# Optimization experiments

Measured on AMD Instinct MI355X. Metric: run time of the kernel, lower is better.

## Reference

```python
import jax, jax.numpy as jnp
import numpy as np

E = 768
NH_REG = 6   # num_heads - cultural_heads
NH_CUL = 2   # cultural_heads


def _branch(x, wq, bq, wk, bk, wv, bv, wo, bo, cb, nh, mask_add):
    # x: [B,T,E]; weights stored as [in,out]; cb: [1,nh,1,hd]
    B, T, Edim = x.shape
    hd = Edim // nh
    scale = hd ** -0.5
    q = (x @ wq + bq).reshape(B, T, nh, hd).transpose(0, 2, 1, 3)
    k = (x @ wk + bk).reshape(B, T, nh, hd).transpose(0, 2, 1, 3)
    v = (x @ wv + bv).reshape(B, T, nh, hd).transpose(0, 2, 1, 3)
    q = q + cb  # learned cultural bias added to Q
    scores = jnp.einsum('bhtd,bhsd->bhts', q, k) * scale
    scores = scores + mask_add
    w = jax.nn.softmax(scores, axis=-1)  # dropout omitted (eval mode)
    out = jnp.einsum('bhts,bhsd->bhtd', w, v)
    out = out.transpose(0, 2, 1, 3).reshape(B, T, Edim)
    return out @ wo + bo


def setup_inputs() -> dict:
    key = jax.random.key(0)
    ks = jax.random.split(key, 24)
    B, S = 2, 2048
    d = {
        'hidden_states': jax.random.normal(ks[0], (B, S, E), jnp.float32),
        'cultural_mask': jax.random.normal(ks[1], (B, S, S), jnp.float32),
        'attention_mask': jax.random.normal(ks[2], (B, 1, 1, S), jnp.float32),
    }
    s = E ** -0.5
    names = ['rq_w', 'rk_w', 'rv_w', 'ro_w', 'cq_w', 'ck_w', 'cv_w', 'co_w']
    for i, n in enumerate(names):
        d[n] = jax.random.normal(ks[3 + i], (E, E), jnp.float32) * s
    for i, n in enumerate(['rq_b', 'rk_b', 'rv_b', 'ro_b', 'cq_b', 'ck_b', 'cv_b', 'co_b']):
        d[n] = jax.random.normal(ks[11 + i], (E,), jnp.float32) * 0.02
    d['r_cb'] = jnp.zeros((1, NH_REG, 1, E // NH_REG), jnp.float32)
    d['c_cb'] = jnp.zeros((1, NH_CUL, 1, E // NH_CUL), jnp.float32)
    # NOTE: concat of two branches gives 2E features -> out layer maps 2E -> E
    d['out_w'] = jax.random.normal(ks[19], (2 * E, E), jnp.float32) * (2 * E) ** -0.5
    d['out_b'] = jax.random.normal(ks[20], (E,), jnp.float32) * 0.02
    return d


def reference(hidden_states, cultural_mask, attention_mask,
              rq_w, rk_w, rv_w, ro_w, cq_w, ck_w, cv_w, co_w,
              rq_b, rk_b, rv_b, ro_b, cq_b, ck_b, cv_b, co_b,
              r_cb, c_cb, out_w, out_b):
    # regular branch: attention_mask only
    reg = _branch(hidden_states, rq_w, rq_b, rk_w, rk_b, rv_w, rv_b,
                  ro_w, ro_b, r_cb, NH_REG, attention_mask)
    # cultural branch: cultural_mask (broadcast over heads) + attention_mask
    cmask = cultural_mask[:, None, :, :] + attention_mask
    cul = _branch(hidden_states, cq_w, cq_b, ck_w, ck_b, cv_w, cv_b,
                  co_w, co_b, c_cb, NH_CUL, cmask)
    combined = jnp.concatenate([reg, cul], axis=-1)  # [B,T,2E]
    return combined @ out_w + out_b
```

## Files before the change

kernel.cpp:

```cpp
#include <hip/hip_runtime.h>
#include <hip/hip_bf16.h>

using u16 = unsigned short;
using u32 = unsigned int;
typedef short short8 __attribute__((ext_vector_type(8)));
typedef float f32x4 __attribute__((ext_vector_type(4)));

#define B_  2
#define S_  2048
#define E_  768
#define BS_ 4096

#define L2E_ 1.44269504088896f
#define FML2_ 17.3123404906676f

__device__ __forceinline__ u16 f2bf(float f) {
  __hip_bfloat16 h = __float2bfloat16(f);
  return *reinterpret_cast<u16*>(&h);
}

__device__ __forceinline__ u32 pk2(float a, float b) {
  return (u32)f2bf(a) | ((u32)f2bf(b) << 16);
}

__device__ __forceinline__ void gld16(const void* g, void* l) {
  __builtin_amdgcn_global_load_lds(
      (const __attribute__((address_space(1))) u32*)g,
      (__attribute__((address_space(3))) u32*)l, 16, 0, 0);
}

__device__ __forceinline__ void stage64(const u16* __restrict__ src, int srcStride,
                                        u16* buf, int w, int lane) {
  const int rl = lane >> 3;
  const int cg0 = lane & 7;
#pragma unroll
  for (int it = 0; it < 4; ++it) {
    int r0 = w * 32 + it * 8;
    int row = r0 + rl;
    int cg = cg0 ^ (row & 7);
    gld16(src + (size_t)row * srcStride + cg * 8, buf + r0 * 64 + lane * 8);
  }
}

__device__ __forceinline__ short8 rdfrag64(const u16* buf, int r, int kt, int quad) {
  int slot = (((kt >> 3) + quad) ^ (r & 7)) & 7;
  return *reinterpret_cast<const short8*>(buf + r * 64 + slot * 8);
}

struct PrepP {
  const float* x;  u16* Xb;
  const float* row; const float* cow; u16* Wrc;
  const float* tsrc[7]; u16* tdst[7]; int trows[7];
  const float* rqb; const float* rkb; const float* rvb;
  const float* cqb; const float* ckb; const float* cvb;
  const float* rcb; const float* ccb;
  float* bqkv; float* bzero;
};

__global__ __launch_bounds__(256) void prep_k(PrepP p) {
  const int bid = blockIdx.x, tid = threadIdx.x;
  __shared__ float tsh[32][33];
  if (bid < 3072) {
    int i = bid * 256 + tid;
    float4 v = reinterpret_cast<const float4*>(p.x)[i];
    reinterpret_cast<uint2*>(p.Xb)[i] = make_uint2(pk2(v.x, v.y), pk2(v.z, v.w));
  } else if (bid < 4224) {
    int i = (bid - 3072) * 256 + tid;
    const float* s = (i < 147456) ? p.row : p.cow;
    int k = (i < 147456) ? i : i - 147456;
    float4 v = reinterpret_cast<const float4*>(s)[k];
    reinterpret_cast<uint2*>(p.Wrc)[i] = make_uint2(pk2(v.x, v.y), pk2(v.z, v.w));
  } else if (bid < 8832) {
    int tb = bid - 4224;
    int mi, ty, tx;
    if (tb < 3456) { mi = tb / 576; int r = tb - mi * 576; ty = r / 24; tx = r - ty * 24; }
    else           { int r = tb - 3456; mi = 6; ty = r / 24; tx = r - ty * 24; }
    const float* src = p.tsrc[mi];
    u16* dst = p.tdst[mi];
    const int rows = p.trows[mi];
    const int r0 = ty * 32, c0 = tx * 32;
    const int txx = tid & 31, tyy = tid >> 5;
#pragma unroll
    for (int d = 0; d < 4; ++d) {
      int r = tyy + d * 8;
      tsh[r][txx] = src[(size_t)(r0 + r) * 768 + c0 + txx];
    }
    __syncthreads();
#pragma unroll
    for (int d = 0; d < 4; ++d) {
      int c = tyy + d * 8;
      dst[(size_t)(c0 + c) * rows + r0 + txx] = f2bf(tsh[txx][c]);
    }
  } else {
    int t = (bid - 8832) * 256 + tid;
    if (t < 4608) {
      int seg = t / 768, i = t - seg * 768;
      float v = 0.f;
      if      (seg == 0) v = p.rqb[i] + p.rcb[i];
      else if (seg == 1) v = p.rkb[i];
      else if (seg == 2) v = p.rvb[i];
      else if (seg == 3) v = p.cqb[i] + p.ccb[i];
      else if (seg == 4) v = p.ckb[i];
      else               v = p.cvb[i];
      p.bqkv[t] = v;
    } else if (t < 6144) {
      p.bzero[t - 4608] = 0.f;
    }
  }
}

__global__ __launch_bounds__(256) void bfused_k(
    const u16* __restrict__ outwT, const float* __restrict__ out_b,
    const float* __restrict__ ro_b, const float* __restrict__ co_b,
    float* __restrict__ bfused) {
  __shared__ float rcb[1536];
  const int tid = threadIdx.x, w = tid >> 6, lane = tid & 63;
  for (int i = tid; i < 768; i += 256) {
    rcb[i] = ro_b[i];
    rcb[768 + i] = co_b[i];
  }
  __syncthreads();
  const int of = blockIdx.x * 4 + w;
  const u16* row = outwT + (size_t)of * 1536 + lane * 24;
  const float* rc = rcb + lane * 24;
  float a0 = 0.f, a1 = 0.f, a2 = 0.f, a3 = 0.f;
#pragma unroll
  for (int g = 0; g < 3; ++g) {
    short8 v = *reinterpret_cast<const short8*>(row + g * 8);
    u32 b0 = ((u32)(u16)v[0]) << 16, b1 = ((u32)(u16)v[1]) << 16;
    u32 b2 = ((u32)(u16)v[2]) << 16, b3 = ((u32)(u16)v[3]) << 16;
    u32 b4 = ((u32)(u16)v[4]) << 16, b5 = ((u32)(u16)v[5]) << 16;
    u32 b6 = ((u32)(u16)v[6]) << 16, b7 = ((u32)(u16)v[7]) << 16;
    a0 = fmaf(*reinterpret_cast<float*>(&b0), rc[g * 8 + 0], a0);
    a1 = fmaf(*reinterpret_cast<float*>(&b1), rc[g * 8 + 1], a1);
    a2 = fmaf(*reinterpret_cast<float*>(&b2), rc[g * 8 + 2], a2);
    a3 = fmaf(*reinterpret_cast<float*>(&b3), rc[g * 8 + 3], a3);
    a0 = fmaf(*reinterpret_cast<float*>(&b4), rc[g * 8 + 4], a0);
    a1 = fmaf(*reinterpret_cast<float*>(&b5), rc[g * 8 + 5], a1);
    a2 = fmaf(*reinterpret_cast<float*>(&b6), rc[g * 8 + 6], a2);
    a3 = fmaf(*reinterpret_cast<float*>(&b7), rc[g * 8 + 7], a3);
  }
  float s = (a0 + a1) + (a2 + a3);
  s += __shfl_xor(s, 1);
  s += __shfl_xor(s, 2);
  s += __shfl_xor(s, 4);
  s += __shfl_xor(s, 8);
  s += __shfl_xor(s, 16);
  s += __shfl_xor(s, 32);
  if (lane == 0) bfused[of] = s + out_b[of];
}


template<int MODE>
__global__ __launch_bounds__(256) void gemm_t_k(
    const u16* __restrict__ A, int lda,
    const u16* __restrict__ BT, int ldb,
    const float* __restrict__ bias, int K,
    const u16* __restrict__ A2, int msplit, int bofs,
    void* __restrict__ Cout, int ldc,
    u16* __restrict__ Qr, u16* __restrict__ Kr, u16* __restrict__ Vtr,
    u16* __restrict__ Qc, u16* __restrict__ Kc, u16* __restrict__ Vtc) {
  __shared__ __align__(16) u16 lA[128 * 64];
  __shared__ __align__(16) u16 lB[128 * 64];
  const int tid = threadIdx.x, w = tid >> 6, lane = tid & 63;
  const int quad = lane >> 4, l15 = lane & 15;
  const int m0 = blockIdx.y * 128, n0 = blockIdx.x * 128;
  if (msplit && m0 >= msplit) { A = A2 - (size_t)msplit * lda; BT += bofs; }

  const f32x4 z4 = {0.f, 0.f, 0.f, 0.f};
  f32x4 acc[4][4];
#pragma unroll
  for (int i = 0; i < 4; ++i)
#pragma unroll
    for (int j = 0; j < 4; ++j) acc[i][j] = z4;

  for (int kc = 0; kc < K; kc += 64) {
    stage64(A + (size_t)m0 * lda + kc, lda, lA, w, lane);
    stage64(BT + (size_t)n0 * ldb + kc, ldb, lB, w, lane);
    __syncthreads();
#pragma unroll
    for (int kt = 0; kt < 64; kt += 32) {
      short8 af[4], bg[4];
#pragma unroll
      for (int i = 0; i < 4; ++i)
        af[i] = rdfrag64(lA, (w >> 1) * 64 + i * 16 + l15, kt, quad);
#pragma unroll
      for (int j = 0; j < 4; ++j)
        bg[j] = rdfrag64(lB, (w & 1) * 64 + j * 16 + l15, kt, quad);
#pragma unroll
      for (int i = 0; i < 4; ++i)
#pragma unroll
        for (int j = 0; j < 4; ++j)
          acc[i][j] = __builtin_amdgcn_mfma_f32_16x16x32_bf16(af[i], bg[j], acc[i][j], 0, 0, 0);
    }
    __syncthreads();
  }

  const int seg = (MODE == 2) ? (m0 / 768) : 0;
#pragma unroll
  for (int i = 0; i < 4; ++i) {
    int f = m0 + (w >> 1) * 64 + i * 16 + quad * 4;
    float4 b4 = *reinterpret_cast<const float4*>(bias + f);
#pragma unroll
    for (int j = 0; j < 4; ++j) {
      int t = n0 + (w & 1) * 64 + j * 16 + l15;
      float v0 = acc[i][j][0] + b4.x;
      float v1 = acc[i][j][1] + b4.y;
      float v2 = acc[i][j][2] + b4.z;
      float v3 = acc[i][j][3] + b4.w;
      if (MODE == 0) {
        *reinterpret_cast<uint2*>((u16*)Cout + (size_t)t * ldc + f) =
            make_uint2(pk2(v0, v1), pk2(v2, v3));
      } else if (MODE == 1) {
        *reinterpret_cast<float4*>((float*)Cout + (size_t)t * ldc + f) =
            make_float4(v0, v1, v2, v3);
      } else {
        int b = t >> 11, s = t & 2047;
        int fs = f - seg * 768;
        if (seg == 0) {
          int h = fs >> 7, d = fs & 127;
          *reinterpret_cast<uint2*>(Qr + ((size_t)(b * 6 + h) * 2048 + s) * 128 + d) =
              make_uint2(pk2(v0, v1), pk2(v2, v3));
        } else if (seg == 1) {
          int h = fs >> 7, d = fs & 127;
          *reinterpret_cast<uint2*>(Kr + ((size_t)(b * 6 + h) * 2048 + s) * 128 + d) =
              make_uint2(pk2(v0, v1), pk2(v2, v3));
        } else if (seg == 2) {
          int h = fs >> 7, d = fs & 127;
          u16* vp = Vtr + ((size_t)(b * 6 + h) * 128 + d) * 2048 + s;
          vp[0] = f2bf(v0); vp[2048] = f2bf(v1); vp[4096] = f2bf(v2); vp[6144] = f2bf(v3);
        } else if (seg == 3) {
          int h = fs / 384, d = fs - h * 384;
          *reinterpret_cast<uint2*>(Qc + ((size_t)(b * 2 + h) * 2048 + s) * 384 + d) =
              make_uint2(pk2(v0, v1), pk2(v2, v3));
        } else if (seg == 4) {
          int h = fs / 384, d = fs - h * 384;
          *reinterpret_cast<uint2*>(Kc + ((size_t)(b * 2 + h) * 2048 + s) * 384 + d) =
              make_uint2(pk2(v0, v1), pk2(v2, v3));
        } else {
          int h = fs / 384, d = fs - h * 384;
          u16* vp = Vtc + ((size_t)(b * 2 + h) * 384 + d) * 2048 + s;
          vp[0] = f2bf(v0); vp[2048] = f2bf(v1); vp[4096] = f2bf(v2); vp[6144] = f2bf(v3);
        }
      }
    }
  }
}

__global__ __launch_bounds__(256) void attn_g1_k(
    const u16* __restrict__ Qr, const u16* __restrict__ Kr,
    const u16* __restrict__ Qc, const u16* __restrict__ Kc,
    u16* __restrict__ Pr, u16* __restrict__ Pc, float* __restrict__ Lp,
    const float* __restrict__ am, const float* __restrict__ cmask,
    float sReg, float sCul, int zoff) {
  __shared__ __align__(16) u16 lA[128 * 64];
  __shared__ __align__(16) u16 lB[128 * 64];
  const int tid = threadIdx.x, w = tid >> 6, lane = tid & 63;
  const int quad = lane >> 4, l15 = lane & 15;
  const int m0 = blockIdx.y * 128, n0 = blockIdx.x * 128;
  const int gz = zoff + blockIdx.z;
  const u16 *A, *BT;
  u16* P;
  const float* cm = nullptr;
  float scl;
  int K, b;
  if (gz < 12) {
    A = Kr + (size_t)gz * S_ * 128;
    BT = Qr + (size_t)gz * S_ * 128;
    K = 128;
    P = Pr + (size_t)blockIdx.z * (size_t)S_ * S_;
    scl = sReg;
    b = gz / 6;
  } else {
    int hc = gz - 12;
    A = Kc + (size_t)hc * S_ * 384;
    BT = Qc + (size_t)hc * S_ * 384;
    K = 384;
    P = Pc + (size_t)hc * (size_t)S_ * S_;
    b = hc >> 1;
    cm = cmask + (size_t)b * S_ * S_;
    scl = sCul;
  }

  const f32x4 z4 = {0.f, 0.f, 0.f, 0.f};
  f32x4 acc[4][4];
#pragma unroll
  for (int i = 0; i < 4; ++i)
#pragma unroll
    for (int j = 0; j < 4; ++j) acc[i][j] = z4;

  for (int kc = 0; kc < K; kc += 64) {
    stage64(A + (size_t)m0 * K + kc, K, lA, w, lane);
    stage64(BT + (size_t)n0 * K + kc, K, lB, w, lane);
    __syncthreads();
#pragma unroll
    for (int kt = 0; kt < 64; kt += 32) {
      short8 af[4], bg[4];
#pragma unroll
      for (int i = 0; i < 4; ++i)
        af[i] = rdfrag64(lA, (w >> 1) * 64 + i * 16 + l15, kt, quad);
#pragma unroll
      for (int j = 0; j < 4; ++j)
        bg[j] = rdfrag64(lB, (w & 1) * 64 + j * 16 + l15, kt, quad);
#pragma unroll
      for (int i = 0; i < 4; ++i)
#pragma unroll
        for (int j = 0; j < 4; ++j)
          acc[i][j] = __builtin_amdgcn_mfma_f32_16x16x32_bf16(af[i], bg[j], acc[i][j], 0, 0, 0);
    }
    __syncthreads();
  }

  const float* amb = am + b * S_;
  float lsum[4] = {0.f, 0.f, 0.f, 0.f};
#pragma unroll
  for (int i = 0; i < 4; ++i) {
    int kb = m0 + (w >> 1) * 64 + i * 16 + quad * 4;
    float4 a4 = *reinterpret_cast<const float4*>(amb + kb);
    float pre0 = fmaf(a4.x, L2E_, -FML2_);
    float pre1 = fmaf(a4.y, L2E_, -FML2_);
    float pre2 = fmaf(a4.z, L2E_, -FML2_);
    float pre3 = fmaf(a4.w, L2E_, -FML2_);
#pragma unroll
    for (int j = 0; j < 4; ++j) {
      int q = n0 + (w & 1) * 64 + j * 16 + l15;
      float c0 = pre0, c1 = pre1, c2 = pre2, c3 = pre3;
      if (cm) {
        float4 cmv = *reinterpret_cast<const float4*>(cm + (size_t)q * S_ + kb);
        c0 = fmaf(cmv.x, L2E_, c0);
        c1 = fmaf(cmv.y, L2E_, c1);
        c2 = fmaf(cmv.z, L2E_, c2);
        c3 = fmaf(cmv.w, L2E_, c3);
      }
      float p0 = exp2f(fmaf(acc[i][j][0], scl, c0));
      float p1 = exp2f(fmaf(acc[i][j][1], scl, c1));
      float p2 = exp2f(fmaf(acc[i][j][2], scl, c2));
      float p3 = exp2f(fmaf(acc[i][j][3], scl, c3));
      lsum[j] += (p0 + p1) + (p2 + p3);
      *reinterpret_cast<uint2*>(P + (size_t)q * S_ + kb) =
          make_uint2(pk2(p0, p1), pk2(p2, p3));
    }
  }
#pragma unroll
  for (int j = 0; j < 4; ++j) {
    float s = lsum[j];
    s += __shfl_xor(s, 16);
    s += __shfl_xor(s, 32);
    if (lane < 16)
      Lp[(size_t)gz * (32 * S_) + ((size_t)((m0 >> 7) * 2 + (w >> 1))) * S_ +
         n0 + (w & 1) * 64 + j * 16 + lane] = s;
  }
}

__global__ __launch_bounds__(256) void attn_g2_k(
    const u16* __restrict__ Pr, const u16* __restrict__ Pc,
    const u16* __restrict__ Vtr, const u16* __restrict__ Vtc,
    const float* __restrict__ Lp, u16* __restrict__ AO, int zoff) {
  const int gz = zoff + blockIdx.z;
  const int m0 = blockIdx.y * 128, n0 = blockIdx.x * 128;
  const u16 *A, *BT;
  int b, colbase;
  if (gz < 12) {
    if (blockIdx.y) return;
    A = Vtr + (size_t)gz * 128 * S_;
    BT = Pr + (size_t)blockIdx.z * (size_t)S_ * S_;
    b = gz / 6;
    colbase = (gz % 6) * 128;
  } else {
    int hc = gz - 12;
    A = Vtc + (size_t)hc * 384 * S_;
    BT = Pc + (size_t)hc * (size_t)S_ * S_;
    b = hc >> 1;
    colbase = 768 + (hc & 1) * 384;
  }
  __shared__ __align__(16) u16 lA[128 * 64];
  __shared__ __align__(16) u16 lB[128 * 64];
  __shared__ float lL[128];
  const int tid = threadIdx.x, w = tid >> 6, lane = tid & 63;
  const int quad = lane >> 4, l15 = lane & 15;

  if (tid < 128) {
    const float* lp = Lp + (size_t)gz * (32 * S_) + (n0 + tid);
    float s = 0.f;
#pragma unroll
    for (int g = 0; g < 32; ++g) s += lp[(size_t)g * S_];
    lL[tid] = 1.f / s;
  }

  const f32x4 z4 = {0.f, 0.f, 0.f, 0.f};
  f32x4 acc[4][4];
#pragma unroll
  for (int i = 0; i < 4; ++i)
#pragma unroll
    for (int j = 0; j < 4; ++j) acc[i][j] = z4;

  for (int kc = 0; kc < S_; kc += 64) {
    stage64(A + (size_t)m0 * S_ + kc, S_, lA, w, lane);
    stage64(BT + (size_t)n0 * S_ + kc, S_, lB, w, lane);
    __syncthreads();
#pragma unroll
    for (int kt = 0; kt < 64; kt += 32) {
      short8 af[4], bg[4];
#pragma unroll
      for (int i = 0; i < 4; ++i)
        af[i] = rdfrag64(lA, (w >> 1) * 64 + i * 16 + l15, kt, quad);
#pragma unroll
      for (int j = 0; j < 4; ++j)
        bg[j] = rdfrag64(lB, (w & 1) * 64 + j * 16 + l15, kt, quad);
#pragma unroll
      for (int i = 0; i < 4; ++i)
#pragma unroll
        for (int j = 0; j < 4; ++j)
          acc[i][j] = __builtin_amdgcn_mfma_f32_16x16x32_bf16(af[i], bg[j], acc[i][j], 0, 0, 0);
    }
    __syncthreads();
  }

  float invl[4];
#pragma unroll
  for (int j = 0; j < 4; ++j) invl[j] = lL[(w & 1) * 64 + j * 16 + l15];
#pragma unroll
  for (int i = 0; i < 4; ++i) {
    int feat = colbase + m0 + (w >> 1) * 64 + i * 16 + quad * 4;
#pragma unroll
    for (int j = 0; j < 4; ++j) {
      int q = n0 + (w & 1) * 64 + j * 16 + l15;
      float v0 = acc[i][j][0] * invl[j];
      float v1 = acc[i][j][1] * invl[j];
      float v2 = acc[i][j][2] * invl[j];
      float v3 = acc[i][j][3] * invl[j];
      *reinterpret_cast<uint2*>(AO + ((size_t)(b * S_ + q)) * 1536 + feat) =
          make_uint2(pk2(v0, v1), pk2(v2, v3));
    }
  }
}


extern "C" void kernel_launch(void* const* d_in, const int* in_sizes, int n_in,
                              void* d_out, int out_size, void* d_ws, size_t ws_size,
                              hipStream_t stream) {
  const float* x     = (const float*)d_in[0];
  const float* cmask = (const float*)d_in[1];
  const float* amask = (const float*)d_in[2];
  const float* W[8]  = { (const float*)d_in[3], (const float*)d_in[4], (const float*)d_in[5],
                         (const float*)d_in[6], (const float*)d_in[7], (const float*)d_in[8],
                         (const float*)d_in[9], (const float*)d_in[10] };
  const float* rq_b = (const float*)d_in[11];
  const float* rk_b = (const float*)d_in[12];
  const float* rv_b = (const float*)d_in[13];
  const float* ro_b = (const float*)d_in[14];
  const float* cq_b = (const float*)d_in[15];
  const float* ck_b = (const float*)d_in[16];
  const float* cv_b = (const float*)d_in[17];
  const float* co_b = (const float*)d_in[18];
  const float* r_cb = (const float*)d_in[19];
  const float* c_cb = (const float*)d_in[20];
  const float* out_w = (const float*)d_in[21];
  const float* out_b = (const float*)d_in[22];

  char* p = (char*)d_ws;
  auto carve = [&](size_t bytes) -> void* {
    void* r = (void*)p;
    p += (bytes + 255) & ~(size_t)255;
    return r;
  };
  u16* Xb    = (u16*)carve((size_t)BS_ * E_ * 2);
  u16* WqkvT = (u16*)carve((size_t)4608 * 768 * 2);
  u16* outwT = (u16*)carve((size_t)768 * 1536 * 2);
  u16* Wrc   = (u16*)carve((size_t)1536 * 768 * 2);
  u16* WfT   = (u16*)carve((size_t)768 * 1536 * 2);
  float* bqkv   = (float*)carve(4608 * 4);
  float* bzero  = (float*)carve(1536 * 4);
  float* bfused = (float*)carve(768 * 4);
  u16* Qr  = (u16*)carve((size_t)B_ * 6 * S_ * 128 * 2);
  u16* Kr  = (u16*)carve((size_t)B_ * 6 * S_ * 128 * 2);
  u16* Vtr = (u16*)carve((size_t)B_ * 6 * S_ * 128 * 2);
  u16* Qc  = (u16*)carve((size_t)B_ * 2 * S_ * 384 * 2);
  u16* Kc  = (u16*)carve((size_t)B_ * 2 * S_ * 384 * 2);
  u16* Vtc = (u16*)carve((size_t)B_ * 2 * S_ * 384 * 2);
  u16* AO  = (u16*)carve((size_t)BS_ * 1536 * 2);

  float* Lp = (float*)Xb;
  u16* Pcul = (u16*)carve((size_t)4 * S_ * S_ * 2);
  size_t used = (size_t)(p - (char*)d_ws);
  size_t rem = (ws_size > used) ? (ws_size - used) : 0;
  int RCH;
  if      (rem >= (size_t)12 * S_ * S_ * 2 + 4096) RCH = 12;
  else if (rem >= (size_t)4  * S_ * S_ * 2 + 4096) RCH = 4;
  else                                             RCH = 2;
  u16* Preg = (u16*)carve((size_t)RCH * S_ * S_ * 2);

  const float sReg = 0.08838834764831845f * L2E_;
  const float sCul = 0.05103103630798288f * L2E_;

  PrepP pp;
  pp.x = x; pp.Xb = Xb;
  pp.row = W[3]; pp.cow = W[7]; pp.Wrc = Wrc;
  const int wsel[6] = {0, 1, 2, 4, 5, 6};
  for (int i = 0; i < 6; ++i) {
    pp.tsrc[i] = W[wsel[i]];
    pp.tdst[i] = WqkvT + (size_t)i * 768 * 768;
    pp.trows[i] = 768;
  }
  pp.tsrc[6] = out_w; pp.tdst[6] = outwT; pp.trows[6] = 1536;
  pp.rqb = rq_b; pp.rkb = rk_b; pp.rvb = rv_b;
  pp.cqb = cq_b; pp.ckb = ck_b; pp.cvb = cv_b;
  pp.rcb = r_cb; pp.ccb = c_cb;
  pp.bqkv = bqkv; pp.bzero = bzero;
  prep_k<<<dim3(8856), 256, 0, stream>>>(pp);

  bfused_k<<<dim3(192), 256, 0, stream>>>(outwT, out_b, ro_b, co_b, bfused);

  gemm_t_k<0><<<dim3(6, 12), 256, 0, stream>>>(
      Wrc, 768, outwT, 1536, bzero, 768,
      Wrc + (size_t)768 * 768, 768, 768, (void*)WfT, 1536,
      nullptr, nullptr, nullptr, nullptr, nullptr, nullptr);

  gemm_t_k<2><<<dim3(32, 36), 256, 0, stream>>>(
      WqkvT, 768, Xb, 768, bqkv, 768,
      (const u16*)nullptr, 0, 0, (void*)nullptr, 0,
      Qr, Kr, Vtr, Qc, Kc, Vtc);

  if (RCH == 12) {
    attn_g1_k<<<dim3(16, 16, 16), 256, 0, stream>>>(
        Qr, Kr, Qc, Kc, Preg, Pcul, Lp, amask, cmask, sReg, sCul, 0);
    attn_g2_k<<<dim3(16, 3, 16), 256, 0, stream>>>(
        Preg, Pcul, Vtr, Vtc, Lp, AO, 0);
  } else {
    attn_g1_k<<<dim3(16, 16, 4), 256, 0, stream>>>(
        Qr, Kr, Qc, Kc, Preg, Pcul, Lp, amask, cmask, sReg, sCul, 12);
    attn_g2_k<<<dim3(16, 3, 4), 256, 0, stream>>>(
        Preg, Pcul, Vtr, Vtc, Lp, AO, 12);
    for (int c = 0; c < 12; c += RCH) {
      attn_g1_k<<<dim3(16, 16, RCH), 256, 0, stream>>>(
          Qr, Kr, Qc, Kc, Preg, Pcul, Lp, amask, cmask, sReg, sCul, c);
      attn_g2_k<<<dim3(16, 1, RCH), 256, 0, stream>>>(
          Preg, Pcul, Vtr, Vtc, Lp, AO, c);
    }
  }

  gemm_t_k<1><<<dim3(32, 6), 256, 0, stream>>>(
      WfT, 1536, AO, 1536, bfused, 1536,
      (const u16*)nullptr, 0, 0, d_out, 768,
      nullptr, nullptr, nullptr, nullptr, nullptr, nullptr);
}
```

Measured before the change: 379.0 us.

## Double-buffer LDS staging in GEMMs and tile the P matrix layout

Adds a double-buffered LDS pipeline to the small GEMMs and the P·V attention kernel, so the next 64-wide K chunk is loaded while MFMAs run on the current one. The probability matrix P is now stored in 128-column key blocks, so each block's rows are contiguous and the P·V kernel reads contiguous 256-byte rows instead of rows strided by S. The MFMA inner loop moves into a shared helper. Double buffering doubles LDS use per block, which may lower occupancy.

```diff
diff --git a/kernel.cpp b/kernel.cpp
--- a/kernel.cpp
+++ b/kernel.cpp
@@ -45,6 +45,26 @@
 __device__ __forceinline__ short8 rdfrag64(const u16* buf, int r, int kt, int quad) {
   int slot = (((kt >> 3) + quad) ^ (r & 7)) & 7;
   return *reinterpret_cast<const short8*>(buf + r * 64 + slot * 8);
+}
+
+__device__ __forceinline__ void mfma_chunk64(const u16* lA, const u16* lB,
+                                             f32x4 (&acc)[4][4],
+                                             int w, int l15, int quad) {
+#pragma unroll
+  for (int kt = 0; kt < 64; kt += 32) {
+    short8 af[4], bg[4];
+#pragma unroll
+    for (int i = 0; i < 4; ++i)
+      af[i] = rdfrag64(lA, (w >> 1) * 64 + i * 16 + l15, kt, quad);
+#pragma unroll
+    for (int j = 0; j < 4; ++j)
+      bg[j] = rdfrag64(lB, (w & 1) * 64 + j * 16 + l15, kt, quad);
+#pragma unroll
+    for (int i = 0; i < 4; ++i)
+#pragma unroll
+      for (int j = 0; j < 4; ++j)
+        acc[i][j] = __builtin_amdgcn_mfma_f32_16x16x32_bf16(af[i], bg[j], acc[i][j], 0, 0, 0);
+  }
 }
 
 struct PrepP {
@@ -151,7 +171,7 @@
 }
 
 
-template<int MODE>
+template<int MODE, int DB>
 __global__ __launch_bounds__(256) void gemm_t_k(
     const u16* __restrict__ A, int lda,
     const u16* __restrict__ BT, int ldb,
@@ -160,8 +180,8 @@
     void* __restrict__ Cout, int ldc,
     u16* __restrict__ Qr, u16* __restrict__ Kr, u16* __restrict__ Vtr,
     u16* __restrict__ Qc, u16* __restrict__ Kc, u16* __restrict__ Vtc) {
-  __shared__ __align__(16) u16 lA[128 * 64];
-  __shared__ __align__(16) u16 lB[128 * 64];
+  __shared__ __align__(16) u16 lA[DB + 1][128 * 64];
+  __shared__ __align__(16) u16 lB[DB + 1][128 * 64];
   const int tid = threadIdx.x, w = tid >> 6, lane = tid & 63;
   const int quad = lane >> 4, l15 = lane & 15;
   const int m0 = blockIdx.y * 128, n0 = blockIdx.x * 128;
@@ -174,26 +194,29 @@
 #pragma unroll
     for (int j = 0; j < 4; ++j) acc[i][j] = z4;
 
-  for (int kc = 0; kc < K; kc += 64) {
-    stage64(A + (size_t)m0 * lda + kc, lda, lA, w, lane);
-    stage64(BT + (size_t)n0 * ldb + kc, ldb, lB, w, lane);
+  if constexpr (DB) {
+    stage64(A + (size_t)m0 * lda, lda, lA[0], w, lane);
+    stage64(BT + (size_t)n0 * ldb, ldb, lB[0], w, lane);
     __syncthreads();
-#pragma unroll
-    for (int kt = 0; kt < 64; kt += 32) {
-      short8 af[4], bg[4];
-#pragma unroll
-      for (int i = 0; i < 4; ++i)
-        af[i] = rdfrag64(lA, (w >> 1) * 64 + i * 16 + l15, kt, quad);
-#pragma unroll
-      for (int j = 0; j < 4; ++j)
-        bg[j] = rdfrag64(lB, (w & 1) * 64 + j * 16 + l15, kt, quad);
-#pragma unroll
-      for (int i = 0; i < 4; ++i)
-#pragma unroll
-        for (int j = 0; j < 4; ++j)
-          acc[i][j] = __builtin_amdgcn_mfma_f32_16x16x32_bf16(af[i], bg[j], acc[i][j], 0, 0, 0);
-    }
-    __syncthreads();
+    int cur = 0;
+    const int nt = K >> 6;
+    for (int t = 0; t < nt; ++t) {
+      if (t + 1 < nt) {
+        stage64(A + (size_t)m0 * lda + (t + 1) * 64, lda, lA[cur ^ 1], w, lane);
+        stage64(BT + (size_t)n0 * ldb + (t + 1) * 64, ldb, lB[cur ^ 1], w, lane);
+      }
+      mfma_chunk64(lA[cur], lB[cur], acc, w, l15, quad);
+      __syncthreads();
+      cur ^= 1;
+    }
+  } else {
+    for (int kc = 0; kc < K; kc += 64) {
+      stage64(A + (size_t)m0 * lda + kc, lda, lA[0], w, lane);
+      stage64(BT + (size_t)n0 * ldb + kc, ldb, lB[0], w, lane);
+      __syncthreads();
+      mfma_chunk64(lA[0], lB[0], acc, w, l15, quad);
+      __syncthreads();
+    }
   }
 
   const int seg = (MODE == 2) ? (m0 / 768) : 0;
@@ -293,29 +316,17 @@
     stage64(A + (size_t)m0 * K + kc, K, lA, w, lane);
     stage64(BT + (size_t)n0 * K + kc, K, lB, w, lane);
     __syncthreads();
-#pragma unroll
-    for (int kt = 0; kt < 64; kt += 32) {
-      short8 af[4], bg[4];
-#pragma unroll
-      for (int i = 0; i < 4; ++i)
-        af[i] = rdfrag64(lA, (w >> 1) * 64 + i * 16 + l15, kt, quad);
-#pragma unroll
-      for (int j = 0; j < 4; ++j)
-        bg[j] = rdfrag64(lB, (w & 1) * 64 + j * 16 + l15, kt, quad);
-#pragma unroll
-      for (int i = 0; i < 4; ++i)
-#pragma unroll
-        for (int j = 0; j < 4; ++j)
-          acc[i][j] = __builtin_amdgcn_mfma_f32_16x16x32_bf16(af[i], bg[j], acc[i][j], 0, 0, 0);
-    }
+    mfma_chunk64(lA, lB, acc, w, l15, quad);
     __syncthreads();
   }
 
+  u16* Pb = P + (size_t)(m0 >> 7) * (S_ * 128);
   const float* amb = am + b * S_;
   float lsum[4] = {0.f, 0.f, 0.f, 0.f};
 #pragma unroll
   for (int i = 0; i < 4; ++i) {
     int kb = m0 + (w >> 1) * 64 + i * 16 + quad * 4;
+    int kbl = kb & 127;
     float4 a4 = *reinterpret_cast<const float4*>(amb + kb);
     float pre0 = fmaf(a4.x, L2E_, -FML2_);
     float pre1 = fmaf(a4.y, L2E_, -FML2_);
@@ -337,7 +348,7 @@
       float p2 = exp2f(fmaf(acc[i][j][2], scl, c2));
       float p3 = exp2f(fmaf(acc[i][j][3], scl, c3));
       lsum[j] += (p0 + p1) + (p2 + p3);
-      *reinterpret_cast<uint2*>(P + (size_t)q * S_ + kb) =
+      *reinterpret_cast<uint2*>(Pb + (size_t)q * 128 + kbl) =
           make_uint2(pk2(p0, p1), pk2(p2, p3));
     }
   }
@@ -373,8 +384,8 @@
     b = hc >> 1;
     colbase = 768 + (hc & 1) * 384;
   }
-  __shared__ __align__(16) u16 lA[128 * 64];
-  __shared__ __align__(16) u16 lB[128 * 64];
+  __shared__ __align__(16) u16 lA[2][128 * 64];
+  __shared__ __align__(16) u16 lB[2][128 * 64];
   __shared__ float lL[128];
   const int tid = threadIdx.x, w = tid >> 6, lane = tid & 63;
   const int quad = lane >> 4, l15 = lane & 15;
@@ -394,26 +405,23 @@
 #pragma unroll
     for (int j = 0; j < 4; ++j) acc[i][j] = z4;
 
-  for (int kc = 0; kc < S_; kc += 64) {
-    stage64(A + (size_t)m0 * S_ + kc, S_, lA, w, lane);
-    stage64(BT + (size_t)n0 * S_ + kc, S_, lB, w, lane);
+  auto psrc = [&](int kc) {
+    return BT + (size_t)(kc >> 7) * (S_ * 128) + (kc & 64) + (size_t)n0 * 128;
+  };
+
+  stage64(A + (size_t)m0 * S_, S_, lA[0], w, lane);
+  stage64(psrc(0), 128, lB[0], w, lane);
+  __syncthreads();
+  int cur = 0;
+  for (int t = 0; t < 32; ++t) {
+    if (t < 31) {
+      int kn = (t + 1) * 64;
+      stage64(A + (size_t)m0 * S_ + kn, S_, lA[cur ^ 1], w, lane);
+      stage64(psrc(kn), 128, lB[cur ^ 1], w, lane);
+    }
+    mfma_chunk64(lA[cur], lB[cur], acc, w, l15, quad);
     __syncthreads();
-#pragma unroll
-    for (int kt = 0; kt < 64; kt += 32) {
-      short8 af[4], bg[4];
-#pragma unroll
-      for (int i = 0; i < 4; ++i)
-        af[i] = rdfrag64(lA, (w >> 1) * 64 + i * 16 + l15, kt, quad);
-#pragma unroll
-      for (int j = 0; j < 4; ++j)
-        bg[j] = rdfrag64(lB, (w & 1) * 64 + j * 16 + l15, kt, quad);
-#pragma unroll
-      for (int i = 0; i < 4; ++i)
-#pragma unroll
-        for (int j = 0; j < 4; ++j)
-          acc[i][j] = __builtin_amdgcn_mfma_f32_16x16x32_bf16(af[i], bg[j], acc[i][j], 0, 0, 0);
-    }
-    __syncthreads();
+    cur ^= 1;
   }
 
   float invl[4];
@@ -511,12 +519,12 @@
 
   bfused_k<<<dim3(192), 256, 0, stream>>>(outwT, out_b, ro_b, co_b, bfused);
 
-  gemm_t_k<0><<<dim3(6, 12), 256, 0, stream>>>(
+  gemm_t_k<0, 1><<<dim3(6, 12), 256, 0, stream>>>(
       Wrc, 768, outwT, 1536, bzero, 768,
       Wrc + (size_t)768 * 768, 768, 768, (void*)WfT, 1536,
       nullptr, nullptr, nullptr, nullptr, nullptr, nullptr);
 
-  gemm_t_k<2><<<dim3(32, 36), 256, 0, stream>>>(
+  gemm_t_k<2, 0><<<dim3(32, 36), 256, 0, stream>>>(
       WqkvT, 768, Xb, 768, bqkv, 768,
       (const u16*)nullptr, 0, 0, (void*)nullptr, 0,
       Qr, Kr, Vtr, Qc, Kc, Vtc);
@@ -539,7 +547,7 @@
     }
   }
 
-  gemm_t_k<1><<<dim3(32, 6), 256, 0, stream>>>(
+  gemm_t_k<1, 1><<<dim3(32, 6), 256, 0, stream>>>(
       WfT, 1536, AO, 1536, bfused, 1536,
       (const u16*)nullptr, 0, 0, d_out, 768,
       nullptr, nullptr, nullptr, nullptr, nullptr, nullptr);
```

New measurement: 382.1 us. No clear change (+0.8%).
